# Kernel optimization log

Hardware: AMD Instinct MI355X
Metric: run time of the kernel (lower is better)

## Reference

```python
import jax, jax.numpy as jnp
import numpy as np

N_NODES = 100000


def sage_conv(x, src, dst, w_self, w_neigh, b):
    # DGL SAGEConv('mean'): h = x @ W_self + mean_{u in N(v)} x_u @ W_neigh + b
    ones = jnp.ones(src.shape[0], dtype=x.dtype)
    deg = jax.ops.segment_sum(ones, dst, num_segments=N_NODES)  # [N]
    neigh_sum = jax.ops.segment_sum(x[src], dst, num_segments=N_NODES)  # [N, F]
    neigh = neigh_sum / jnp.clip(deg, 1.0)[:, None]  # isolated nodes -> 0
    return x @ w_self + neigh @ w_neigh + b


def setup_inputs() -> dict:
    key = jax.random.key(0)
    ks = jax.random.split(key, 9)
    nfeat, nhid, nclass = 128, 128, 2
    E = 1600000
    x = jax.random.normal(ks[0], (N_NODES, nfeat), dtype=jnp.float32)
    src = jax.random.randint(ks[1], (E,), 0, N_NODES)
    dst = jax.random.randint(ks[2], (E,), 0, N_NODES)
    s1 = 1.0 / np.sqrt(nfeat)
    s2 = 1.0 / np.sqrt(nhid)
    return {
        "x": x,
        "src": src,
        "dst": dst,
        "w_self1": jax.random.uniform(ks[3], (nfeat, nhid), jnp.float32, -s1, s1),
        "w_neigh1": jax.random.uniform(ks[4], (nfeat, nhid), jnp.float32, -s1, s1),
        "b1": jnp.zeros((nhid,), jnp.float32),
        "w_self2": jax.random.uniform(ks[5], (nhid, nclass), jnp.float32, -s2, s2),
        "w_neigh2": jax.random.uniform(ks[6], (nhid, nclass), jnp.float32, -s2, s2),
        "b2": jnp.zeros((nclass,), jnp.float32),
    }


def reference(x, src, dst, w_self1, w_neigh1, b1, w_self2, w_neigh2, b2):
    h = jax.nn.relu(sage_conv(x, src, dst, w_self1, w_neigh1, b1))
    h = sage_conv(h, src, dst, w_self2, w_neigh2, b2)
    return jax.nn.log_softmax(h, axis=1)
```

## Files before the change

### kernel.cpp

```cpp
#include <hip/hip_runtime.h>
#include <hip/hip_bf16.h>


#define N_FEAT 128
#define CSHIFT 9
#define CNODES 512
#define NBINS 256
#define CCAP 9728
#define BATCH 4096
#define BF_BLOCKS 256
#define PW_BLOCKS 128

typedef __attribute__((ext_vector_type(8))) short short8;
typedef __attribute__((ext_vector_type(8))) unsigned short ushort8_t;
typedef __attribute__((ext_vector_type(16))) float f32x16;

__device__ __forceinline__ float bf16_bits_to_f32(ushort u) {
    union { unsigned int i; float f; } c;
    c.i = ((unsigned int)u) << 16;
    return c.f;
}

__global__ __launch_bounds__(256) void prep_and_split_kernel(
    const int* __restrict__ src, const int* __restrict__ dst,
    int* __restrict__ ccursor, unsigned* __restrict__ cbuf, int E,
    const float* __restrict__ x, ushort* __restrict__ xb, int n4,
    const float* __restrict__ w1, const float* __restrict__ w2,
    ushort* __restrict__ wt, int nms) {
    __shared__ unsigned stage[BATCH];
    __shared__ int cntw[4][NBINS];
    __shared__ int curw[4][NBINS];
    __shared__ int excl[NBINS];
    __shared__ int incl[NBINS];
    __shared__ int gpos[NBINS];
    __shared__ int wsum[4];
    int tid = threadIdx.x;
    int bid = blockIdx.x;

    if (bid >= nms) {
        int rb = bid - nms;
        if (rb < BF_BLOCKS) {
            int i = rb * 256 + tid;
            int stride = BF_BLOCKS * 256;
            for (; i < n4; i += stride) {
                float4 v = ((const float4*)x)[i];
                ushort4 r;
                r.x = __bfloat16_as_ushort(__float2bfloat16(v.x));
                r.y = __bfloat16_as_ushort(__float2bfloat16(v.y));
                r.z = __bfloat16_as_ushort(__float2bfloat16(v.z));
                r.w = __bfloat16_as_ushort(__float2bfloat16(v.w));
                ((ushort4*)xb)[i] = r;
            }
        } else {
            int id = (rb - BF_BLOCKS) * 256 + tid;
            int nn = id >> 8;
            int k = id & 255;
            float v = (k < 128) ? w1[k * 128 + nn] : w2[(k - 128) * 128 + nn];
            wt[nn * 256 + k] = __bfloat16_as_ushort(__float2bfloat16(v));
        }
        return;
    }

    int wv = tid >> 6;
    int lane = tid & 63;
    int base = bid * BATCH;
    int total = min(BATCH, E - base);

    unsigned pk[16];
    int bn[16];
    for (int i = tid; i < 4 * NBINS; i += 256) ((int*)cntw)[i] = 0;
    __syncthreads();
    #pragma unroll
    for (int k = 0; k < 16; ++k) {
        int e = base + k * 256 + tid;
        if (e < E) {
            int d = dst[e];
            int sv = src[e];
            bn[k] = d >> CSHIFT;
            pk[k] = ((unsigned)(d & (CNODES - 1)) << 17) | (unsigned)sv;
            atomicAdd(&cntw[wv][bn[k]], 1);
        } else {
            bn[k] = -1;
        }
    }
    __syncthreads();
    int c0 = cntw[0][tid], c1 = cntw[1][tid], c2 = cntw[2][tid], c3 = cntw[3][tid];
    cntw[0][tid] = 0;
    cntw[1][tid] = c0;
    cntw[2][tid] = c0 + c1;
    cntw[3][tid] = c0 + c1 + c2;
    int c = c0 + c1 + c2 + c3;
    int val = c;
    #pragma unroll
    for (int off = 1; off < 64; off <<= 1) {
        int t = __shfl_up(val, off);
        if (lane >= off) val += t;
    }
    if (lane == 63) wsum[wv] = val;
    __syncthreads();
    #pragma unroll
    for (int i = 0; i < 4; ++i)
        if (i < wv) val += wsum[i];
    incl[tid] = val;
    int e0 = val - c;
    excl[tid] = e0;
    curw[0][tid] = e0 + cntw[0][tid];
    curw[1][tid] = e0 + cntw[1][tid];
    curw[2][tid] = e0 + cntw[2][tid];
    curw[3][tid] = e0 + cntw[3][tid];
    gpos[tid] = (c > 0) ? atomicAdd(&ccursor[tid], c) : 0;
    __syncthreads();
    #pragma unroll
    for (int k = 0; k < 16; ++k) {
        if (bn[k] >= 0) {
            int ofs = atomicAdd(&curw[wv][bn[k]], 1);
            stage[ofs] = pk[k];
        }
    }
    __syncthreads();
    for (int i = tid; i < total; i += 256) {
        int lo = 0, hi = NBINS - 1;
        while (lo < hi) {
            int mid = (lo + hi) >> 1;
            if (incl[mid] > i) hi = mid; else lo = mid + 1;
        }
        int b = lo;
        int target = gpos[b] + (i - excl[b]);
        cbuf[(size_t)b * CCAP + target] = stage[i];
    }
}

__global__ __launch_bounds__(512) void build_csr2_kernel(
    const unsigned* __restrict__ cbuf, const int* __restrict__ ccnt,
    int* __restrict__ row_ptr, int* __restrict__ csr, int N, int E) {
    __shared__ int hist[CNODES];
    __shared__ int cur[CNODES];
    __shared__ int wred[8];
    __shared__ int cstart_s;
    int cb = blockIdx.x;
    int tid = threadIdx.x;
    int lane = tid & 63;
    int w = tid >> 6;

    int v = (tid < cb) ? ccnt[tid] : 0;
    #pragma unroll
    for (int off = 32; off > 0; off >>= 1) v += __shfl_xor(v, off);
    if (lane == 0) wred[w] = v;
    hist[tid] = 0;
    __syncthreads();
    if (tid == 0) {
        int t = 0;
        #pragma unroll
        for (int i = 0; i < 8; ++i) t += wred[i];
        cstart_s = t;
    }
    if (cb == 0 && tid == 0) row_ptr[N] = E;
    int cnt = ccnt[cb];
    size_t bbase = (size_t)cb * CCAP;
    __syncthreads();
    int base = cstart_s;

    for (int e = tid; e < cnt; e += 512) {
        unsigned p = cbuf[bbase + e];
        atomicAdd(&hist[p >> 17], 1);
    }
    __syncthreads();
    int c = hist[tid];
    int val = c;
    #pragma unroll
    for (int off = 1; off < 64; off <<= 1) {
        int t = __shfl_up(val, off);
        if (lane >= off) val += t;
    }
    if (lane == 63) wred[w] = val;
    __syncthreads();
    #pragma unroll
    for (int i = 0; i < 8; ++i)
        if (i < w) val += wred[i];
    int excl = val - c;
    int node = cb * CNODES + tid;
    if (node < N) row_ptr[node] = base + excl;
    cur[tid] = excl;
    __syncthreads();
    for (int e = tid; e < cnt; e += 512) {
        unsigned p = cbuf[bbase + e];
        int bin = p >> 17;
        int ofs = atomicAdd(&cur[bin], 1);
        csr[base + ofs] = (int)(p & 0x1FFFF);
    }
}

__global__ __launch_bounds__(256) void aggregate_bf16_kernel(
    const ushort* __restrict__ xb, const int* __restrict__ row_ptr,
    const int* __restrict__ csr, ushort* __restrict__ out, int n) {
    int v = blockIdx.x * 4 + (threadIdx.x >> 6);
    int lane = threadIdx.x & 63;
    int sub = lane >> 4;
    int fc = lane & 15;
    if (v >= n) return;
    int beg = row_ptr[v];
    int end = row_ptr[v + 1];
    float acc[8];
    #pragma unroll
    for (int j = 0; j < 8; ++j) acc[j] = 0.f;
    const ushort* xfc = xb + fc * 8;
    int e = beg;
    for (; e + 16 <= end; e += 16) {
        int s0 = csr[e + sub];
        int s1 = csr[e + 4 + sub];
        int s2 = csr[e + 8 + sub];
        int s3 = csr[e + 12 + sub];
        ushort8_t t0 = *(const ushort8_t*)(xfc + (size_t)s0 * N_FEAT);
        ushort8_t t1 = *(const ushort8_t*)(xfc + (size_t)s1 * N_FEAT);
        ushort8_t t2 = *(const ushort8_t*)(xfc + (size_t)s2 * N_FEAT);
        ushort8_t t3 = *(const ushort8_t*)(xfc + (size_t)s3 * N_FEAT);
        #pragma unroll
        for (int j = 0; j < 8; ++j) acc[j] += bf16_bits_to_f32(t0[j]);
        #pragma unroll
        for (int j = 0; j < 8; ++j) acc[j] += bf16_bits_to_f32(t1[j]);
        #pragma unroll
        for (int j = 0; j < 8; ++j) acc[j] += bf16_bits_to_f32(t2[j]);
        #pragma unroll
        for (int j = 0; j < 8; ++j) acc[j] += bf16_bits_to_f32(t3[j]);
    }
    if (e + 8 <= end) {
        int s0 = csr[e + sub];
        int s1 = csr[e + 4 + sub];
        ushort8_t t0 = *(const ushort8_t*)(xfc + (size_t)s0 * N_FEAT);
        ushort8_t t1 = *(const ushort8_t*)(xfc + (size_t)s1 * N_FEAT);
        #pragma unroll
        for (int j = 0; j < 8; ++j) acc[j] += bf16_bits_to_f32(t0[j]);
        #pragma unroll
        for (int j = 0; j < 8; ++j) acc[j] += bf16_bits_to_f32(t1[j]);
        e += 8;
    }
    if (e + 4 <= end) {
        int s0 = csr[e + sub];
        ushort8_t t0 = *(const ushort8_t*)(xfc + (size_t)s0 * N_FEAT);
        #pragma unroll
        for (int j = 0; j < 8; ++j) acc[j] += bf16_bits_to_f32(t0[j]);
        e += 4;
    }
    int rem = end - e;
    if (sub < rem) {
        int s0 = csr[e + sub];
        ushort8_t t0 = *(const ushort8_t*)(xfc + (size_t)s0 * N_FEAT);
        #pragma unroll
        for (int j = 0; j < 8; ++j) acc[j] += bf16_bits_to_f32(t0[j]);
    }
    #pragma unroll
    for (int j = 0; j < 8; ++j) {
        acc[j] += __shfl_xor(acc[j], 16);
        acc[j] += __shfl_xor(acc[j], 32);
    }
    if (lane < 16) {
        int deg = end - beg;
        float inv = (deg > 0) ? 1.0f / (float)deg : 0.0f;
        ushort8_t r;
        #pragma unroll
        for (int j = 0; j < 8; ++j)
            r[j] = __bfloat16_as_ushort(__float2bfloat16(acc[j] * inv));
        *(ushort8_t*)(out + (size_t)v * N_FEAT + lane * 8) = r;
    }
}

__global__ __launch_bounds__(256) void gemm1_fused_kernel(
    const ushort* __restrict__ xb, const ushort* __restrict__ nbb,
    const ushort* __restrict__ wt, const float* __restrict__ b,
    const float* __restrict__ ws2, const float* __restrict__ wn2,
    float* __restrict__ s_out, float* __restrict__ z_out, int n) {
    __shared__ ushort As[128 * 72];
    __shared__ ushort Bs[128 * 72];
    int tid = threadIdx.x;
    int wave = tid >> 6;
    int lane = tid & 63;
    int m = lane & 31;
    int half = lane >> 5;
    int block_row = blockIdx.x * 128;

    f32x16 acc[4];
    #pragma unroll
    for (int t = 0; t < 4; ++t)
        #pragma unroll
        for (int i = 0; i < 16; ++i) acc[t][i] = 0.0f;

    for (int kc = 0; kc < 4; ++kc) {
        const ushort* A = (kc < 2) ? xb : nbb;
        int k0 = (kc & 1) * 64;
        #pragma unroll
        for (int l = 0; l < 4; ++l) {
            int idx = l * 256 + tid;
            int r = idx >> 3;
            int p = idx & 7;
            int node = block_row + r;
            ushort8_t v;
            if (node < n) {
                v = *(const ushort8_t*)(A + (size_t)node * N_FEAT + k0 + p * 8);
            } else {
                #pragma unroll
                for (int q = 0; q < 8; ++q) v[q] = 0;
            }
            *(ushort8_t*)(&As[r * 72 + p * 8]) = v;
        }
        #pragma unroll
        for (int l = 0; l < 4; ++l) {
            int idx = l * 256 + tid;
            int cc = idx >> 3;
            int p = idx & 7;
            ushort8_t v = *(const ushort8_t*)(wt + (size_t)cc * 256 + kc * 64 + p * 8);
            *(ushort8_t*)(&Bs[cc * 72 + p * 8]) = v;
        }
        __syncthreads();
        #pragma unroll
        for (int ks = 0; ks < 4; ++ks) {
            int koff = ks * 16 + half * 8;
            short8 a = *(const short8*)(&As[(32 * wave + m) * 72 + koff]);
            short8 bf0 = *(const short8*)(&Bs[(0 * 32 + m) * 72 + koff]);
            short8 bf1 = *(const short8*)(&Bs[(1 * 32 + m) * 72 + koff]);
            short8 bf2 = *(const short8*)(&Bs[(2 * 32 + m) * 72 + koff]);
            short8 bf3 = *(const short8*)(&Bs[(3 * 32 + m) * 72 + koff]);
            acc[0] = __builtin_amdgcn_mfma_f32_32x32x16_bf16(a, bf0, acc[0], 0, 0, 0);
            acc[1] = __builtin_amdgcn_mfma_f32_32x32x16_bf16(a, bf1, acc[1], 0, 0, 0);
            acc[2] = __builtin_amdgcn_mfma_f32_32x32x16_bf16(a, bf2, acc[2], 0, 0, 0);
            acc[3] = __builtin_amdgcn_mfma_f32_32x32x16_bf16(a, bf3, acc[3], 0, 0, 0);
        }
        __syncthreads();
    }

    float bcol[4], wsc[4][2], wnc[4][2];
    #pragma unroll
    for (int t = 0; t < 4; ++t) {
        int col = t * 32 + m;
        bcol[t] = b[col];
        float2 a = ((const float2*)ws2)[col];
        float2 q = ((const float2*)wn2)[col];
        wsc[t][0] = a.x; wsc[t][1] = a.y;
        wnc[t][0] = q.x; wnc[t][1] = q.y;
    }
    #pragma unroll
    for (int reg = 0; reg < 16; ++reg) {
        int rowin = (reg & 3) + 8 * (reg >> 2) + 4 * half;
        int node = block_row + 32 * wave + rowin;
        float p0 = 0.f, p1 = 0.f, q0 = 0.f, q1 = 0.f;
        #pragma unroll
        for (int t = 0; t < 4; ++t) {
            float hv = fmaxf(acc[t][reg] + bcol[t], 0.0f);
            p0 += hv * wsc[t][0]; p1 += hv * wsc[t][1];
            q0 += hv * wnc[t][0]; q1 += hv * wnc[t][1];
        }
        #pragma unroll
        for (int off = 1; off < 32; off <<= 1) {
            p0 += __shfl_xor(p0, off);
            p1 += __shfl_xor(p1, off);
            q0 += __shfl_xor(q0, off);
            q1 += __shfl_xor(q1, off);
        }
        if (m == 0 && node < n) {
            ((float2*)s_out)[node] = make_float2(p0, p1);
            ((float2*)z_out)[node] = make_float2(q0, q1);
        }
    }
}

__global__ void layer2b_kernel(const float* __restrict__ s_in, const float* __restrict__ z,
                               const int* __restrict__ row_ptr, const int* __restrict__ csr,
                               const float* __restrict__ b, float* __restrict__ out, int n) {
    int v = blockIdx.x * 256 + threadIdx.x;
    if (v >= n) return;
    int beg = row_ptr[v];
    int end = row_ptr[v + 1];
    float a0 = 0.f, a1 = 0.f, c0 = 0.f, c1 = 0.f;
    int e = beg;
    for (; e + 2 <= end; e += 2) {
        float2 t0 = ((const float2*)z)[csr[e]];
        float2 t1 = ((const float2*)z)[csr[e + 1]];
        a0 += t0.x; a1 += t0.y;
        c0 += t1.x; c1 += t1.y;
    }
    if (e < end) {
        float2 t0 = ((const float2*)z)[csr[e]];
        a0 += t0.x; a1 += t0.y;
    }
    int deg = end - beg;
    float inv = (deg > 0) ? 1.0f / (float)deg : 0.0f;
    float2 sv = ((const float2*)s_in)[v];
    float o0 = sv.x + (a0 + c0) * inv + b[0];
    float o1 = sv.y + (a1 + c1) * inv + b[1];
    float mx = fmaxf(o0, o1);
    float lse = mx + logf(expf(o0 - mx) + expf(o1 - mx));
    ((float2*)out)[v] = make_float2(o0 - lse, o1 - lse);
}

extern "C" void kernel_launch(void* const* d_in, const int* in_sizes, int n_in,
                              void* d_out, int out_size, void* d_ws, size_t ws_size,
                              hipStream_t stream) {
    const float* x        = (const float*)d_in[0];
    const int*   src      = (const int*)d_in[1];
    const int*   dst      = (const int*)d_in[2];
    const float* w_self1  = (const float*)d_in[3];
    const float* w_neigh1 = (const float*)d_in[4];
    const float* b1       = (const float*)d_in[5];
    const float* w_self2  = (const float*)d_in[6];
    const float* w_neigh2 = (const float*)d_in[7];
    const float* b2       = (const float*)d_in[8];
    float* out = (float*)d_out;

    int N = in_sizes[0] / N_FEAT;
    int E = in_sizes[1];
    int nbk = (N + CNODES - 1) / CNODES;
    int nms = (E + BATCH - 1) / BATCH;

    char* ws = (char*)d_ws;
    size_t off = 0;
    auto alloc = [&](size_t bytes) -> void* {
        void* p = ws + off;
        off += (bytes + 255) & ~(size_t)255;
        return p;
    };
    int*      ccursor = (int*)alloc(NBINS * 4);
    int*      row_ptr = (int*)alloc((size_t)(N + 1) * 4);
    int*      csr     = (int*)alloc((size_t)E * 4);
    unsigned* cbuf    = (unsigned*)alloc((size_t)nbk * CCAP * 4);
    ushort*   xb      = (ushort*)alloc((size_t)N * N_FEAT * 2);
    ushort*   nbb     = (ushort*)alloc((size_t)N * N_FEAT * 2);
    ushort*   wt      = (ushort*)alloc((size_t)128 * 256 * 2);
    float*    s_buf   = (float*)alloc((size_t)N * 2 * 4);
    float*    z_buf   = (float*)alloc((size_t)N * 2 * 4);
    (void)ws_size; (void)n_in; (void)out_size;

    hipMemsetAsync(ccursor, 0, NBINS * 4, stream);

    prep_and_split_kernel<<<nms + BF_BLOCKS + PW_BLOCKS, 256, 0, stream>>>(
        src, dst, ccursor, cbuf, E, x, xb, N * N_FEAT / 4, w_self1, w_neigh1, wt, nms);
    build_csr2_kernel<<<nbk, 512, 0, stream>>>(cbuf, ccursor, row_ptr, csr, N, E);
    aggregate_bf16_kernel<<<(N + 3) / 4, 256, 0, stream>>>(xb, row_ptr, csr, nbb, N);
    gemm1_fused_kernel<<<(N + 127) / 128, 256, 0, stream>>>(
        xb, nbb, wt, b1, w_self2, w_neigh2, s_buf, z_buf, N);
    layer2b_kernel<<<(N + 255) / 256, 256, 0, stream>>>(s_buf, z_buf, row_ptr, csr, b2, out, N);
}
```

Baseline: 244.6 us.

## Fuse neighbor mean aggregation into layer-1 GEMM kernel via shared memory

Aggregation of neighbor features now happens inside the GEMM kernel: each wave gathers and averages 32 nodes' neighbors into an LDS tile, which then feeds the MFMA loop directly. This removes the intermediate bf16 neighbor-mean buffer, its global write and re-read, and one kernel launch. In exchange, the block count drops sharply, LDS use per block grows, and each wave processes nodes serially, reducing latency hiding for the irregular gather.

```diff
diff --git a/kernel.cpp b/kernel.cpp
--- a/kernel.cpp
+++ b/kernel.cpp
@@ -190,117 +190,118 @@
     }
 }
 
-__global__ __launch_bounds__(256) void aggregate_bf16_kernel(
+__global__ __launch_bounds__(256) void agg_gemm_kernel(
     const ushort* __restrict__ xb, const int* __restrict__ row_ptr,
-    const int* __restrict__ csr, ushort* __restrict__ out, int n) {
-    int v = blockIdx.x * 4 + (threadIdx.x >> 6);
-    int lane = threadIdx.x & 63;
-    int sub = lane >> 4;
-    int fc = lane & 15;
-    if (v >= n) return;
-    int beg = row_ptr[v];
-    int end = row_ptr[v + 1];
-    float acc[8];
-    #pragma unroll
-    for (int j = 0; j < 8; ++j) acc[j] = 0.f;
-    const ushort* xfc = xb + fc * 8;
-    int e = beg;
-    for (; e + 16 <= end; e += 16) {
-        int s0 = csr[e + sub];
-        int s1 = csr[e + 4 + sub];
-        int s2 = csr[e + 8 + sub];
-        int s3 = csr[e + 12 + sub];
-        ushort8_t t0 = *(const ushort8_t*)(xfc + (size_t)s0 * N_FEAT);
-        ushort8_t t1 = *(const ushort8_t*)(xfc + (size_t)s1 * N_FEAT);
-        ushort8_t t2 = *(const ushort8_t*)(xfc + (size_t)s2 * N_FEAT);
-        ushort8_t t3 = *(const ushort8_t*)(xfc + (size_t)s3 * N_FEAT);
-        #pragma unroll
-        for (int j = 0; j < 8; ++j) acc[j] += bf16_bits_to_f32(t0[j]);
-        #pragma unroll
-        for (int j = 0; j < 8; ++j) acc[j] += bf16_bits_to_f32(t1[j]);
-        #pragma unroll
-        for (int j = 0; j < 8; ++j) acc[j] += bf16_bits_to_f32(t2[j]);
-        #pragma unroll
-        for (int j = 0; j < 8; ++j) acc[j] += bf16_bits_to_f32(t3[j]);
-    }
-    if (e + 8 <= end) {
-        int s0 = csr[e + sub];
-        int s1 = csr[e + 4 + sub];
-        ushort8_t t0 = *(const ushort8_t*)(xfc + (size_t)s0 * N_FEAT);
-        ushort8_t t1 = *(const ushort8_t*)(xfc + (size_t)s1 * N_FEAT);
-        #pragma unroll
-        for (int j = 0; j < 8; ++j) acc[j] += bf16_bits_to_f32(t0[j]);
-        #pragma unroll
-        for (int j = 0; j < 8; ++j) acc[j] += bf16_bits_to_f32(t1[j]);
-        e += 8;
-    }
-    if (e + 4 <= end) {
-        int s0 = csr[e + sub];
-        ushort8_t t0 = *(const ushort8_t*)(xfc + (size_t)s0 * N_FEAT);
-        #pragma unroll
-        for (int j = 0; j < 8; ++j) acc[j] += bf16_bits_to_f32(t0[j]);
-        e += 4;
-    }
-    int rem = end - e;
-    if (sub < rem) {
-        int s0 = csr[e + sub];
-        ushort8_t t0 = *(const ushort8_t*)(xfc + (size_t)s0 * N_FEAT);
-        #pragma unroll
-        for (int j = 0; j < 8; ++j) acc[j] += bf16_bits_to_f32(t0[j]);
-    }
-    #pragma unroll
-    for (int j = 0; j < 8; ++j) {
-        acc[j] += __shfl_xor(acc[j], 16);
-        acc[j] += __shfl_xor(acc[j], 32);
-    }
-    if (lane < 16) {
-        int deg = end - beg;
-        float inv = (deg > 0) ? 1.0f / (float)deg : 0.0f;
-        ushort8_t r;
-        #pragma unroll
-        for (int j = 0; j < 8; ++j)
-            r[j] = __bfloat16_as_ushort(__float2bfloat16(acc[j] * inv));
-        *(ushort8_t*)(out + (size_t)v * N_FEAT + lane * 8) = r;
-    }
-}
-
-__global__ __launch_bounds__(256) void gemm1_fused_kernel(
-    const ushort* __restrict__ xb, const ushort* __restrict__ nbb,
-    const ushort* __restrict__ wt, const float* __restrict__ b,
-    const float* __restrict__ ws2, const float* __restrict__ wn2,
-    float* __restrict__ s_out, float* __restrict__ z_out, int n) {
+    const int* __restrict__ csr, const ushort* __restrict__ wt,
+    const float* __restrict__ b, const float* __restrict__ ws2,
+    const float* __restrict__ wn2, float* __restrict__ s_out,
+    float* __restrict__ z_out, int n) {
     __shared__ ushort As[128 * 72];
     __shared__ ushort Bs[128 * 72];
+    __shared__ ushort Ns[128 * 136];
     int tid = threadIdx.x;
     int wave = tid >> 6;
     int lane = tid & 63;
     int m = lane & 31;
     int half = lane >> 5;
     int block_row = blockIdx.x * 128;
-
-    f32x16 acc[4];
+    int base_node = block_row + 32 * wave;
+
+    int sub = lane >> 4;
+    int fc = lane & 15;
+    const ushort* xfc = xb + fc * 8;
+    int rp = 0;
+    if (lane < 33) rp = row_ptr[min(base_node + lane, n)];
+    for (int i = 0; i < 32; ++i) {
+        int beg = __shfl(rp, i);
+        int end = __shfl(rp, i + 1);
+        float acc[8];
+        #pragma unroll
+        for (int j = 0; j < 8; ++j) acc[j] = 0.f;
+        int e = beg;
+        for (; e + 16 <= end; e += 16) {
+            int s0 = csr[e + sub];
+            int s1 = csr[e + 4 + sub];
+            int s2 = csr[e + 8 + sub];
+            int s3 = csr[e + 12 + sub];
+            ushort8_t t0 = *(const ushort8_t*)(xfc + (size_t)s0 * N_FEAT);
+            ushort8_t t1 = *(const ushort8_t*)(xfc + (size_t)s1 * N_FEAT);
+            ushort8_t t2 = *(const ushort8_t*)(xfc + (size_t)s2 * N_FEAT);
+            ushort8_t t3 = *(const ushort8_t*)(xfc + (size_t)s3 * N_FEAT);
+            #pragma unroll
+            for (int j = 0; j < 8; ++j) acc[j] += bf16_bits_to_f32(t0[j]);
+            #pragma unroll
+            for (int j = 0; j < 8; ++j) acc[j] += bf16_bits_to_f32(t1[j]);
+            #pragma unroll
+            for (int j = 0; j < 8; ++j) acc[j] += bf16_bits_to_f32(t2[j]);
+            #pragma unroll
+            for (int j = 0; j < 8; ++j) acc[j] += bf16_bits_to_f32(t3[j]);
+        }
+        if (e + 8 <= end) {
+            int s0 = csr[e + sub];
+            int s1 = csr[e + 4 + sub];
+            ushort8_t t0 = *(const ushort8_t*)(xfc + (size_t)s0 * N_FEAT);
+            ushort8_t t1 = *(const ushort8_t*)(xfc + (size_t)s1 * N_FEAT);
+            #pragma unroll
+            for (int j = 0; j < 8; ++j) acc[j] += bf16_bits_to_f32(t0[j]);
+            #pragma unroll
+            for (int j = 0; j < 8; ++j) acc[j] += bf16_bits_to_f32(t1[j]);
+            e += 8;
+        }
+        if (e + 4 <= end) {
+            int s0 = csr[e + sub];
+            ushort8_t t0 = *(const ushort8_t*)(xfc + (size_t)s0 * N_FEAT);
+            #pragma unroll
+            for (int j = 0; j < 8; ++j) acc[j] += bf16_bits_to_f32(t0[j]);
+            e += 4;
+        }
+        int rem = end - e;
+        if (sub < rem) {
+            int s0 = csr[e + sub];
+            ushort8_t t0 = *(const ushort8_t*)(xfc + (size_t)s0 * N_FEAT);
+            #pragma unroll
+            for (int j = 0; j < 8; ++j) acc[j] += bf16_bits_to_f32(t0[j]);
+        }
+        #pragma unroll
+        for (int j = 0; j < 8; ++j) {
+            acc[j] += __shfl_xor(acc[j], 16);
+            acc[j] += __shfl_xor(acc[j], 32);
+        }
+        if (lane < 16) {
+            int deg = end - beg;
+            float inv = (deg > 0) ? 1.0f / (float)deg : 0.0f;
+            ushort8_t r;
+            #pragma unroll
+            for (int j = 0; j < 8; ++j)
+                r[j] = __bfloat16_as_ushort(__float2bfloat16(acc[j] * inv));
+            *(ushort8_t*)(&Ns[(32 * wave + i) * 136 + fc * 8]) = r;
+        }
+    }
+
+    f32x16 acc4[4];
     #pragma unroll
     for (int t = 0; t < 4; ++t)
         #pragma unroll
-        for (int i = 0; i < 16; ++i) acc[t][i] = 0.0f;
+        for (int i = 0; i < 16; ++i) acc4[t][i] = 0.0f;
 
     for (int kc = 0; kc < 4; ++kc) {
-        const ushort* A = (kc < 2) ? xb : nbb;
-        int k0 = (kc & 1) * 64;
-        #pragma unroll
-        for (int l = 0; l < 4; ++l) {
-            int idx = l * 256 + tid;
-            int r = idx >> 3;
-            int p = idx & 7;
-            int node = block_row + r;
-            ushort8_t v;
-            if (node < n) {
-                v = *(const ushort8_t*)(A + (size_t)node * N_FEAT + k0 + p * 8);
-            } else {
-                #pragma unroll
-                for (int q = 0; q < 8; ++q) v[q] = 0;
+        if (kc < 2) {
+            int k0 = kc * 64;
+            #pragma unroll
+            for (int l = 0; l < 4; ++l) {
+                int idx = l * 256 + tid;
+                int r = idx >> 3;
+                int p = idx & 7;
+                int node = block_row + r;
+                ushort8_t v;
+                if (node < n) {
+                    v = *(const ushort8_t*)(xb + (size_t)node * N_FEAT + k0 + p * 8);
+                } else {
+                    #pragma unroll
+                    for (int q = 0; q < 8; ++q) v[q] = 0;
+                }
+                *(ushort8_t*)(&As[r * 72 + p * 8]) = v;
             }
-            *(ushort8_t*)(&As[r * 72 + p * 8]) = v;
         }
         #pragma unroll
         for (int l = 0; l < 4; ++l) {
@@ -314,15 +315,19 @@
         #pragma unroll
         for (int ks = 0; ks < 4; ++ks) {
             int koff = ks * 16 + half * 8;
-            short8 a = *(const short8*)(&As[(32 * wave + m) * 72 + koff]);
+            short8 a;
+            if (kc < 2)
+                a = *(const short8*)(&As[(32 * wave + m) * 72 + koff]);
+            else
+                a = *(const short8*)(&Ns[(32 * wave + m) * 136 + (kc - 2) * 64 + koff]);
             short8 bf0 = *(const short8*)(&Bs[(0 * 32 + m) * 72 + koff]);
             short8 bf1 = *(const short8*)(&Bs[(1 * 32 + m) * 72 + koff]);
             short8 bf2 = *(const short8*)(&Bs[(2 * 32 + m) * 72 + koff]);
             short8 bf3 = *(const short8*)(&Bs[(3 * 32 + m) * 72 + koff]);
-            acc[0] = __builtin_amdgcn_mfma_f32_32x32x16_bf16(a, bf0, acc[0], 0, 0, 0);
-            acc[1] = __builtin_amdgcn_mfma_f32_32x32x16_bf16(a, bf1, acc[1], 0, 0, 0);
-            acc[2] = __builtin_amdgcn_mfma_f32_32x32x16_bf16(a, bf2, acc[2], 0, 0, 0);
-            acc[3] = __builtin_amdgcn_mfma_f32_32x32x16_bf16(a, bf3, acc[3], 0, 0, 0);
+            acc4[0] = __builtin_amdgcn_mfma_f32_32x32x16_bf16(a, bf0, acc4[0], 0, 0, 0);
+            acc4[1] = __builtin_amdgcn_mfma_f32_32x32x16_bf16(a, bf1, acc4[1], 0, 0, 0);
+            acc4[2] = __builtin_amdgcn_mfma_f32_32x32x16_bf16(a, bf2, acc4[2], 0, 0, 0);
+            acc4[3] = __builtin_amdgcn_mfma_f32_32x32x16_bf16(a, bf3, acc4[3], 0, 0, 0);
         }
         __syncthreads();
     }
@@ -344,7 +349,7 @@
         float p0 = 0.f, p1 = 0.f, q0 = 0.f, q1 = 0.f;
         #pragma unroll
         for (int t = 0; t < 4; ++t) {
-            float hv = fmaxf(acc[t][reg] + bcol[t], 0.0f);
+            float hv = fmaxf(acc4[t][reg] + bcol[t], 0.0f);
             p0 += hv * wsc[t][0]; p1 += hv * wsc[t][1];
             q0 += hv * wnc[t][0]; q1 += hv * wnc[t][1];
         }
@@ -422,7 +427,6 @@
     int*      csr     = (int*)alloc((size_t)E * 4);
     unsigned* cbuf    = (unsigned*)alloc((size_t)nbk * CCAP * 4);
     ushort*   xb      = (ushort*)alloc((size_t)N * N_FEAT * 2);
-    ushort*   nbb     = (ushort*)alloc((size_t)N * N_FEAT * 2);
     ushort*   wt      = (ushort*)alloc((size_t)128 * 256 * 2);
     float*    s_buf   = (float*)alloc((size_t)N * 2 * 4);
     float*    z_buf   = (float*)alloc((size_t)N * 2 * 4);
@@ -433,8 +437,7 @@
     prep_and_split_kernel<<<nms + BF_BLOCKS + PW_BLOCKS, 256, 0, stream>>>(
         src, dst, ccursor, cbuf, E, x, xb, N * N_FEAT / 4, w_self1, w_neigh1, wt, nms);
     build_csr2_kernel<<<nbk, 512, 0, stream>>>(cbuf, ccursor, row_ptr, csr, N, E);
-    aggregate_bf16_kernel<<<(N + 3) / 4, 256, 0, stream>>>(xb, row_ptr, csr, nbb, N);
-    gemm1_fused_kernel<<<(N + 127) / 128, 256, 0, stream>>>(
-        xb, nbb, wt, b1, w_self2, w_neigh2, s_buf, z_buf, N);
+    agg_gemm_kernel<<<(N + 127) / 128, 256, 0, stream>>>(
+        xb, row_ptr, csr, wt, b1, w_self2, w_neigh2, s_buf, z_buf, N);
     layer2b_kernel<<<(N + 255) / 256, 256, 0, stream>>>(s_buf, z_buf, row_ptr, csr, b2, out, N);
 }
```

New measurement: 302.1 us. 23.5% more time.

## Project features by W_neigh before aggregation and add neighbor term in GEMM epilogue

Applied to the files above, without the earlier changes.

Reorders layer-1 math so x @ W_neigh is computed first (new MFMA blocks in the prep kernel writing yb), then the mean aggregation runs over the projected features, and gemm1 only does the self half (K=128) and adds the aggregated term elementwise in its epilogue. This halves the GEMM K dimension and removes the second A-tile load stream. In exchange it adds an extra N×128 GEMM pass and a bf16 buffer write, the epilogue now does scattered per-element 2-byte loads of nbb, and the rounding point of the neighbour term changes because the projection is rounded to bf16 before averaging.

```diff
diff --git a/kernel.cpp b/kernel.cpp
--- a/kernel.cpp
+++ b/kernel.cpp
@@ -20,22 +20,21 @@
     c.i = ((unsigned int)u) << 16;
     return c.f;
 }
+__device__ __forceinline__ ushort f32_to_bf16_bits(float f) {
+    return __bfloat16_as_ushort(__float2bfloat16(f));
+}
 
 __global__ __launch_bounds__(256) void prep_and_split_kernel(
     const int* __restrict__ src, const int* __restrict__ dst,
     int* __restrict__ ccursor, unsigned* __restrict__ cbuf, int E,
     const float* __restrict__ x, ushort* __restrict__ xb, int n4,
-    const float* __restrict__ w1, const float* __restrict__ w2,
-    ushort* __restrict__ wt, int nms) {
-    __shared__ unsigned stage[BATCH];
-    __shared__ int cntw[4][NBINS];
-    __shared__ int curw[4][NBINS];
-    __shared__ int excl[NBINS];
-    __shared__ int incl[NBINS];
-    __shared__ int gpos[NBINS];
-    __shared__ int wsum[4];
+    const float* __restrict__ w1, const float* __restrict__ wn1,
+    ushort* __restrict__ wt, ushort* __restrict__ yb, int n, int nms) {
+    __shared__ __align__(16) char smem[36864];
     int tid = threadIdx.x;
     int bid = blockIdx.x;
+    int wave = tid >> 6;
+    int lane = tid & 63;
 
     if (bid >= nms) {
         int rb = bid - nms;
@@ -45,30 +44,109 @@
             for (; i < n4; i += stride) {
                 float4 v = ((const float4*)x)[i];
                 ushort4 r;
-                r.x = __bfloat16_as_ushort(__float2bfloat16(v.x));
-                r.y = __bfloat16_as_ushort(__float2bfloat16(v.y));
-                r.z = __bfloat16_as_ushort(__float2bfloat16(v.z));
-                r.w = __bfloat16_as_ushort(__float2bfloat16(v.w));
+                r.x = f32_to_bf16_bits(v.x);
+                r.y = f32_to_bf16_bits(v.y);
+                r.z = f32_to_bf16_bits(v.z);
+                r.w = f32_to_bf16_bits(v.w);
                 ((ushort4*)xb)[i] = r;
             }
-        } else {
+        } else if (rb < BF_BLOCKS + PW_BLOCKS) {
             int id = (rb - BF_BLOCKS) * 256 + tid;
             int nn = id >> 8;
             int k = id & 255;
-            float v = (k < 128) ? w1[k * 128 + nn] : w2[(k - 128) * 128 + nn];
-            wt[nn * 256 + k] = __bfloat16_as_ushort(__float2bfloat16(v));
+            float v = (k < 128) ? w1[k * 128 + nn] : wn1[(k - 128) * 128 + nn];
+            wt[nn * 256 + k] = f32_to_bf16_bits(v);
+        } else {
+            int rb2 = rb - BF_BLOCKS - PW_BLOCKS;
+            int block_row = rb2 * 128;
+            int m = lane & 31;
+            int half = lane >> 5;
+            ushort* As = (ushort*)smem;
+            ushort* Bs = (ushort*)(smem + 18432);
+            f32x16 acc[4];
+            #pragma unroll
+            for (int t = 0; t < 4; ++t)
+                #pragma unroll
+                for (int i = 0; i < 16; ++i) acc[t][i] = 0.0f;
+            for (int kc = 0; kc < 2; ++kc) {
+                int k0 = kc * 64;
+                #pragma unroll
+                for (int l = 0; l < 4; ++l) {
+                    int idx = l * 256 + tid;
+                    int r = idx >> 3;
+                    int p = idx & 7;
+                    int node = block_row + r;
+                    ushort8_t v;
+                    if (node < n) {
+                        const float* xp = x + (size_t)node * N_FEAT + k0 + p * 8;
+                        float4 f0 = *(const float4*)xp;
+                        float4 f1 = *(const float4*)(xp + 4);
+                        v[0] = f32_to_bf16_bits(f0.x); v[1] = f32_to_bf16_bits(f0.y);
+                        v[2] = f32_to_bf16_bits(f0.z); v[3] = f32_to_bf16_bits(f0.w);
+                        v[4] = f32_to_bf16_bits(f1.x); v[5] = f32_to_bf16_bits(f1.y);
+                        v[6] = f32_to_bf16_bits(f1.z); v[7] = f32_to_bf16_bits(f1.w);
+                    } else {
+                        #pragma unroll
+                        for (int q = 0; q < 8; ++q) v[q] = 0;
+                    }
+                    *(ushort8_t*)(&As[r * 72 + p * 8]) = v;
+                }
+                #pragma unroll
+                for (int l = 0; l < 4; ++l) {
+                    int idx = l * 256 + tid;
+                    int cc = idx >> 3;
+                    int p = idx & 7;
+                    ushort8_t v;
+                    #pragma unroll
+                    for (int j = 0; j < 8; ++j)
+                        v[j] = f32_to_bf16_bits(wn1[(size_t)(k0 + p * 8 + j) * 128 + cc]);
+                    *(ushort8_t*)(&Bs[cc * 72 + p * 8]) = v;
+                }
+                __syncthreads();
+                #pragma unroll
+                for (int ks = 0; ks < 4; ++ks) {
+                    int koff = ks * 16 + half * 8;
+                    short8 a = *(const short8*)(&As[(32 * wave + m) * 72 + koff]);
+                    short8 bf0 = *(const short8*)(&Bs[(0 * 32 + m) * 72 + koff]);
+                    short8 bf1 = *(const short8*)(&Bs[(1 * 32 + m) * 72 + koff]);
+                    short8 bf2 = *(const short8*)(&Bs[(2 * 32 + m) * 72 + koff]);
+                    short8 bf3 = *(const short8*)(&Bs[(3 * 32 + m) * 72 + koff]);
+                    acc[0] = __builtin_amdgcn_mfma_f32_32x32x16_bf16(a, bf0, acc[0], 0, 0, 0);
+                    acc[1] = __builtin_amdgcn_mfma_f32_32x32x16_bf16(a, bf1, acc[1], 0, 0, 0);
+                    acc[2] = __builtin_amdgcn_mfma_f32_32x32x16_bf16(a, bf2, acc[2], 0, 0, 0);
+                    acc[3] = __builtin_amdgcn_mfma_f32_32x32x16_bf16(a, bf3, acc[3], 0, 0, 0);
+                }
+                __syncthreads();
+            }
+            #pragma unroll
+            for (int t = 0; t < 4; ++t) {
+                int col = t * 32 + m;
+                #pragma unroll
+                for (int reg = 0; reg < 16; ++reg) {
+                    int rowin = (reg & 3) + 8 * (reg >> 2) + 4 * half;
+                    int node = block_row + 32 * wave + rowin;
+                    if (node < n)
+                        yb[(size_t)node * N_FEAT + col] = f32_to_bf16_bits(acc[t][reg]);
+                }
+            }
         }
         return;
     }
 
-    int wv = tid >> 6;
-    int lane = tid & 63;
+    unsigned* stage = (unsigned*)smem;
+    int* cntw = (int*)(smem + 16384);
+    int* curw = (int*)(smem + 20480);
+    int* excl = (int*)(smem + 24576);
+    int* incl = (int*)(smem + 25600);
+    int* gpos = (int*)(smem + 26624);
+    int* wsum = (int*)(smem + 27648);
+    int wv = wave;
     int base = bid * BATCH;
     int total = min(BATCH, E - base);
 
     unsigned pk[16];
     int bn[16];
-    for (int i = tid; i < 4 * NBINS; i += 256) ((int*)cntw)[i] = 0;
+    for (int i = tid; i < 4 * NBINS; i += 256) cntw[i] = 0;
     __syncthreads();
     #pragma unroll
     for (int k = 0; k < 16; ++k) {
@@ -78,17 +156,18 @@
             int sv = src[e];
             bn[k] = d >> CSHIFT;
             pk[k] = ((unsigned)(d & (CNODES - 1)) << 17) | (unsigned)sv;
-            atomicAdd(&cntw[wv][bn[k]], 1);
+            atomicAdd(&cntw[wv * NBINS + bn[k]], 1);
         } else {
             bn[k] = -1;
         }
     }
     __syncthreads();
-    int c0 = cntw[0][tid], c1 = cntw[1][tid], c2 = cntw[2][tid], c3 = cntw[3][tid];
-    cntw[0][tid] = 0;
-    cntw[1][tid] = c0;
-    cntw[2][tid] = c0 + c1;
-    cntw[3][tid] = c0 + c1 + c2;
+    int c0 = cntw[0 * NBINS + tid], c1 = cntw[1 * NBINS + tid];
+    int c2 = cntw[2 * NBINS + tid], c3 = cntw[3 * NBINS + tid];
+    cntw[0 * NBINS + tid] = 0;
+    cntw[1 * NBINS + tid] = c0;
+    cntw[2 * NBINS + tid] = c0 + c1;
+    cntw[3 * NBINS + tid] = c0 + c1 + c2;
     int c = c0 + c1 + c2 + c3;
     int val = c;
     #pragma unroll
@@ -104,16 +183,16 @@
     incl[tid] = val;
     int e0 = val - c;
     excl[tid] = e0;
-    curw[0][tid] = e0 + cntw[0][tid];
-    curw[1][tid] = e0 + cntw[1][tid];
-    curw[2][tid] = e0 + cntw[2][tid];
-    curw[3][tid] = e0 + cntw[3][tid];
+    curw[0 * NBINS + tid] = e0 + cntw[0 * NBINS + tid];
+    curw[1 * NBINS + tid] = e0 + cntw[1 * NBINS + tid];
+    curw[2 * NBINS + tid] = e0 + cntw[2 * NBINS + tid];
+    curw[3 * NBINS + tid] = e0 + cntw[3 * NBINS + tid];
     gpos[tid] = (c > 0) ? atomicAdd(&ccursor[tid], c) : 0;
     __syncthreads();
     #pragma unroll
     for (int k = 0; k < 16; ++k) {
         if (bn[k] >= 0) {
-            int ofs = atomicAdd(&curw[wv][bn[k]], 1);
+            int ofs = atomicAdd(&curw[wv * NBINS + bn[k]], 1);
             stage[ofs] = pk[k];
         }
     }
@@ -191,7 +270,7 @@
 }
 
 __global__ __launch_bounds__(256) void aggregate_bf16_kernel(
-    const ushort* __restrict__ xb, const int* __restrict__ row_ptr,
+    const ushort* __restrict__ yb, const int* __restrict__ row_ptr,
     const int* __restrict__ csr, ushort* __restrict__ out, int n) {
     int v = blockIdx.x * 4 + (threadIdx.x >> 6);
     int lane = threadIdx.x & 63;
@@ -203,7 +282,7 @@
     float acc[8];
     #pragma unroll
     for (int j = 0; j < 8; ++j) acc[j] = 0.f;
-    const ushort* xfc = xb + fc * 8;
+    const ushort* xfc = yb + fc * 8;
     int e = beg;
     for (; e + 16 <= end; e += 16) {
         int s0 = csr[e + sub];
@@ -259,7 +338,7 @@
         ushort8_t r;
         #pragma unroll
         for (int j = 0; j < 8; ++j)
-            r[j] = __bfloat16_as_ushort(__float2bfloat16(acc[j] * inv));
+            r[j] = f32_to_bf16_bits(acc[j] * inv);
         *(ushort8_t*)(out + (size_t)v * N_FEAT + lane * 8) = r;
     }
 }
@@ -284,9 +363,8 @@
         #pragma unroll
         for (int i = 0; i < 16; ++i) acc[t][i] = 0.0f;
 
-    for (int kc = 0; kc < 4; ++kc) {
-        const ushort* A = (kc < 2) ? xb : nbb;
-        int k0 = (kc & 1) * 64;
+    for (int kc = 0; kc < 2; ++kc) {
+        int k0 = kc * 64;
         #pragma unroll
         for (int l = 0; l < 4; ++l) {
             int idx = l * 256 + tid;
@@ -295,7 +373,7 @@
             int node = block_row + r;
             ushort8_t v;
             if (node < n) {
-                v = *(const ushort8_t*)(A + (size_t)node * N_FEAT + k0 + p * 8);
+                v = *(const ushort8_t*)(xb + (size_t)node * N_FEAT + k0 + p * 8);
             } else {
                 #pragma unroll
                 for (int q = 0; q < 8; ++q) v[q] = 0;
@@ -341,10 +419,13 @@
     for (int reg = 0; reg < 16; ++reg) {
         int rowin = (reg & 3) + 8 * (reg >> 2) + 4 * half;
         int node = block_row + 32 * wave + rowin;
+        int nd = (node < n) ? node : (n - 1);
         float p0 = 0.f, p1 = 0.f, q0 = 0.f, q1 = 0.f;
         #pragma unroll
         for (int t = 0; t < 4; ++t) {
-            float hv = fmaxf(acc[t][reg] + bcol[t], 0.0f);
+            int col = t * 32 + m;
+            float nb = bf16_bits_to_f32(nbb[(size_t)nd * N_FEAT + col]);
+            float hv = fmaxf(acc[t][reg] + nb + bcol[t], 0.0f);
             p0 += hv * wsc[t][0]; p1 += hv * wsc[t][1];
             q0 += hv * wnc[t][0]; q1 += hv * wnc[t][1];
         }
@@ -409,6 +490,7 @@
     int E = in_sizes[1];
     int nbk = (N + CNODES - 1) / CNODES;
     int nms = (E + BATCH - 1) / BATCH;
+    int nyg = (N + 127) / 128;
 
     char* ws = (char*)d_ws;
     size_t off = 0;
@@ -422,6 +504,7 @@
     int*      csr     = (int*)alloc((size_t)E * 4);
     unsigned* cbuf    = (unsigned*)alloc((size_t)nbk * CCAP * 4);
     ushort*   xb      = (ushort*)alloc((size_t)N * N_FEAT * 2);
+    ushort*   yb      = (ushort*)alloc((size_t)N * N_FEAT * 2);
     ushort*   nbb     = (ushort*)alloc((size_t)N * N_FEAT * 2);
     ushort*   wt      = (ushort*)alloc((size_t)128 * 256 * 2);
     float*    s_buf   = (float*)alloc((size_t)N * 2 * 4);
@@ -430,10 +513,10 @@
 
     hipMemsetAsync(ccursor, 0, NBINS * 4, stream);
 
-    prep_and_split_kernel<<<nms + BF_BLOCKS + PW_BLOCKS, 256, 0, stream>>>(
-        src, dst, ccursor, cbuf, E, x, xb, N * N_FEAT / 4, w_self1, w_neigh1, wt, nms);
+    prep_and_split_kernel<<<nms + BF_BLOCKS + PW_BLOCKS + nyg, 256, 0, stream>>>(
+        src, dst, ccursor, cbuf, E, x, xb, N * N_FEAT / 4, w_self1, w_neigh1, wt, yb, N, nms);
     build_csr2_kernel<<<nbk, 512, 0, stream>>>(cbuf, ccursor, row_ptr, csr, N, E);
-    aggregate_bf16_kernel<<<(N + 3) / 4, 256, 0, stream>>>(xb, row_ptr, csr, nbb, N);
+    aggregate_bf16_kernel<<<(N + 3) / 4, 256, 0, stream>>>(yb, row_ptr, csr, nbb, N);
     gemm1_fused_kernel<<<(N + 127) / 128, 256, 0, stream>>>(
         xb, nbb, wt, b1, w_self2, w_neigh2, s_buf, z_buf, N);
     layer2b_kernel<<<(N + 255) / 256, 256, 0, stream>>>(s_buf, z_buf, row_ptr, csr, b2, out, N);
```

After: 254.5 us. +4.0%, slower.
